# Kernel tuning notes

Measured on AMD Instinct MI355X. Metric: run time of the kernel, lower is better.

## Reference

```python
import jax, jax.numpy as jnp
import numpy as np

NUM_LEVEL = 4

def setup_inputs() -> dict:
    key = jax.random.key(0)
    k1, k2, k3, k4, k5 = jax.random.split(key, 5)
    B, L1, L2, F, H = 8, 1024, 1024, 1024, 1024
    x1_att = jax.random.normal(k1, (B, L1, F), dtype=jnp.float32)
    x2_att = jax.random.normal(k2, (B, L2, F), dtype=jnp.float32)
    x2 = jax.random.normal(k3, (B, L2, H), dtype=jnp.float32)
    x2_mask = jax.random.uniform(k4, (B, L2)) < 0.1
    x2_mask = x2_mask.at[:, 0].set(False)
    W = jax.random.normal(k5, (H, F), dtype=jnp.float32) * 0.02  # nn.Linear weight [out,in]
    final_v = jnp.ones((1, H), dtype=jnp.float32)  # linear_final parameter
    return {"x1_att": x1_att, "x2_att": x2_att, "x2": x2, "x2_mask": x2_mask, "W": W, "final_v": final_v}

def reference(x1_att, x2_att, x2, x2_mask, W, final_v):
    B, L1, F = x1_att.shape
    L2 = x2_att.shape[1]
    H = W.shape[0]
    nl = NUM_LEVEL
    d = H // nl
    # shared linear projection + ReLU (dropout is identity at p=0 / eval)
    x1_key = jax.nn.relu(jnp.einsum('blf,hf->blh', x1_att, W))            # [B,L1,H]
    x2_key = jax.nn.relu(jnp.einsum('blf,hf->blh', x2_att, W)) * final_v  # [B,L2,H]
    x1_rep = x1_key.reshape(B, L1, nl, d)
    x2_rep = x2_key.reshape(B, L2, nl, d)
    # per-level QK^T scores: [B, nl, L1, L2]
    scores = jnp.einsum('bimd,bjmd->bmij', x1_rep, x2_rep)
    scores = jnp.where(x2_mask[:, None, None, :], -jnp.inf, scores)
    alpha = jax.nn.softmax(scores, axis=-1)
    v = x2.reshape(B, L2, nl, d)
    out = jnp.einsum('bmij,bjmd->bimd', alpha, v)  # [B,L1,nl,d]
    return out.reshape(B, L1, H)
```

## Files before the change

kernel.cpp:

```cpp
#include <hip/hip_runtime.h>
#include <hip/hip_bf16.h>
#include <stdint.h>

typedef unsigned short u16;
typedef _Float16 f16_t;
typedef f16_t f16x8 __attribute__((ext_vector_type(8)));
typedef u16 u16x8 __attribute__((ext_vector_type(8)));
typedef u16 u16x4 __attribute__((ext_vector_type(4)));
typedef float f32x4 __attribute__((ext_vector_type(4)));

#define L2E 1.44269504088896f
#define DEFER_THR 7.0f

__device__ __forceinline__ u16 f2h(float f) {
  f16_t h = (f16_t)f;
  return __builtin_bit_cast(u16, h);
}
__device__ __forceinline__ f32x4 mfma16h(u16x8 a, u16x8 b, f32x4 c) {
  return __builtin_amdgcn_mfma_f32_16x16x32_f16(
      __builtin_bit_cast(f16x8, a), __builtin_bit_cast(f16x8, b), c, 0, 0, 0);
}
__device__ __forceinline__ void gl16(const u16 *g, u16 *l) {
  __builtin_amdgcn_global_load_lds(
      (const __attribute__((address_space(1))) void *)g,
      (__attribute__((address_space(3))) void *)l, 16, 0, 0);
}

__global__ void prep_mask_kernel(const unsigned char *__restrict__ mraw,
                                 float *__restrict__ bias) {
  __shared__ int flag;
  int t = threadIdx.x;
  if (t == 0) flag = 0;
  __syncthreads();
  int local = 0;
  for (int i = t; i < 8192; i += 256)
    if ((i & 3) && mraw[i]) local = 1;
  if (local) atomicOr(&flag, 1);
  __syncthreads();
  const bool bytes = (flag != 0);
  const int *mi = (const int *)mraw;
  for (int i = t; i < 8192; i += 256) {
    int m = bytes ? (int)mraw[i] : mi[i];
    bias[i] = m ? -1e30f : 0.0f;
  }
}

__global__ void cvt_f16_kernel(const float *__restrict__ in,
                               u16 *__restrict__ out) {
  int i = (blockIdx.x * 256 + threadIdx.x) * 8;
  f32x4 a = *(const f32x4 *)(in + i);
  f32x4 b = *(const f32x4 *)(in + i + 4);
  u16x8 o;
#pragma unroll
  for (int e = 0; e < 4; ++e) {
    o[e] = f2h(a[e]);
    o[4 + e] = f2h(b[e]);
  }
  *(u16x8 *)(out + i) = o;
}

__global__ void transpose_v_kernel(const float *__restrict__ x2,
                                   u16 *__restrict__ vT) {
  __shared__ float tile[32][33];
  const int b = blockIdx.z, h0 = blockIdx.y * 32, j0 = blockIdx.x * 32;
  const int tx = threadIdx.x & 31, ty = threadIdx.x >> 5;
#pragma unroll
  for (int rr = 0; rr < 32; rr += 8)
    tile[ty + rr][tx] = x2[((size_t)b * 1024 + j0 + ty + rr) * 1024 + h0 + tx];
  __syncthreads();
  const int mlev = h0 >> 8, dd0 = h0 & 255;
#pragma unroll
  for (int rr = 0; rr < 32; rr += 8) {
    int dd = dd0 + ty + rr;
    vT[((size_t)(b * 4 + mlev) * 256 + dd) * 1024 + j0 + tx] =
        f2h(tile[tx][ty + rr]);
  }
}

__global__ __launch_bounds__(256, 2) void proj_kernel(
    const u16 *__restrict__ Ag, const u16 *__restrict__ Bg,
    const float *__restrict__ fv, u16 *__restrict__ outk, int usefv) {
  __shared__ u16 As[2][128 * 32], Bs[2][128 * 32];
  const int t = threadIdx.x;
  const int lane = t & 63, wid = t >> 6;
  const int l16 = lane & 15, g = lane >> 4;
  const int wr = wid >> 1, wc = wid & 1;
  const int bm = blockIdx.x, bn = blockIdx.y;

  f32x4 acc[4][4] = {};

  const int rA0 = 32 * wid + (lane >> 2), rA1 = rA0 + 16;
  const int cA0 = (lane & 3) ^ ((rA0 >> 1) & 3);
  const int cA1 = (lane & 3) ^ ((rA1 >> 1) & 3);
  const u16 *srcA0 = Ag + (size_t)(bm * 128 + rA0) * 1024 + cA0 * 8;
  const u16 *srcA1 = Ag + (size_t)(bm * 128 + rA1) * 1024 + cA1 * 8;
  const u16 *srcB0 = Bg + (size_t)(bn * 128 + rA0) * 1024 + cA0 * 8;
  const u16 *srcB1 = Bg + (size_t)(bn * 128 + rA1) * 1024 + cA1 * 8;
  const int dst0 = wid * 1024, dst1 = wid * 1024 + 512;

  gl16(srcA0, &As[0][dst0]);
  gl16(srcA1, &As[0][dst1]);
  gl16(srcB0, &Bs[0][dst0]);
  gl16(srcB1, &Bs[0][dst1]);

  for (int k0 = 0; k0 < 32; ++k0) {
    const int cur = k0 & 1;
    if (k0 < 31) {
      const int kel = (k0 + 1) * 32, nb = cur ^ 1;
      gl16(srcA0 + kel, &As[nb][dst0]);
      gl16(srcA1 + kel, &As[nb][dst1]);
      gl16(srcB0 + kel, &Bs[nb][dst0]);
      gl16(srcB1 + kel, &Bs[nb][dst1]);
      asm volatile("s_waitcnt vmcnt(4)" ::: "memory");
    } else {
      asm volatile("s_waitcnt vmcnt(0)" ::: "memory");
    }
    __builtin_amdgcn_s_barrier();
    asm volatile("" ::: "memory");

    u16x8 af[4], bf[4];
#pragma unroll
    for (int mf = 0; mf < 4; ++mf) {
      int r = wr * 64 + mf * 16 + l16;
      af[mf] = *(const u16x8 *)(&As[cur][0] + r * 32 + ((g ^ ((r >> 1) & 3)) * 8));
    }
#pragma unroll
    for (int nf = 0; nf < 4; ++nf) {
      int r = wc * 64 + nf * 16 + l16;
      bf[nf] = *(const u16x8 *)(&Bs[cur][0] + r * 32 + ((g ^ ((r >> 1) & 3)) * 8));
    }
    __builtin_amdgcn_s_setprio(1);
#pragma unroll
    for (int mf = 0; mf < 4; ++mf)
#pragma unroll
      for (int nf = 0; nf < 4; ++nf)
        acc[mf][nf] = mfma16h(af[mf], bf[nf], acc[mf][nf]);
    __builtin_amdgcn_s_setprio(0);
    asm volatile("" ::: "memory");
    __builtin_amdgcn_s_barrier();
  }

#pragma unroll
  for (int nf = 0; nf < 4; ++nf) {
    int col = bn * 128 + wc * 64 + nf * 16 + l16;
    float f = usefv ? fv[col] : 1.0f;
#pragma unroll
    for (int mf = 0; mf < 4; ++mf) {
      int row0 = bm * 128 + wr * 64 + mf * 16 + g * 4;
#pragma unroll
      for (int q = 0; q < 4; ++q) {
        float v = acc[mf][nf][q];
        v = (v > 0.f ? v : 0.f) * f;
        outk[(size_t)(row0 + q) * 1024 + col] = f2h(v);
      }
    }
  }
}

__global__ __launch_bounds__(256, 2) void attn_kernel(
    const u16 *__restrict__ x1k, const u16 *__restrict__ x2k,
    const u16 *__restrict__ vT, const float *__restrict__ bias,
    float *__restrict__ out) {
  __shared__ u16 K2s[64 * 256];
  __shared__ u16 VTs[256 * 64];
  __shared__ float biasS[1024];
  __shared__ u16 P[4][16 * 72];

  const int t = threadIdx.x;
  const int lane = t & 63, wid = t >> 6;
  const int l16 = lane & 15, g = lane >> 4;
  const int id = blockIdx.x;
  const int xcd = id & 7, idx = id >> 3;
  const int it = idx & 15, pp = idx >> 4;
  const int pair = xcd + 8 * pp;
  const int b = pair >> 2, m = pair & 3;

  for (int j = t; j < 1024; j += 256) biasS[j] = bias[b * 1024 + j];

  const int qrow = it * 64 + wid * 16 + l16;
  const u16 *qsrc = x1k + ((size_t)b * 1024 + qrow) * 1024 + m * 256;
  u16x8 Q[8];
#pragma unroll
  for (int dk = 0; dk < 8; ++dk) Q[dk] = *(const u16x8 *)(qsrc + dk * 32 + g * 8);

  f32x4 acc[16] = {};
  float mrow[4] = {-1e30f, -1e30f, -1e30f, -1e30f};
  float lrow[4] = {0.f, 0.f, 0.f, 0.f};

  const int sj = t >> 2, cb = (t & 3) * 8;
  const u16 *ksrc = x2k + ((size_t)b * 1024 + sj) * 1024 + m * 256 + cb * 8;
  const u16 *vtsrc = vT + ((size_t)((b * 4 + m) * 256 + t)) * 1024;
  uint32_t koff[8], voff[8];
#pragma unroll
  for (int q = 0; q < 8; ++q) {
    koff[q] = sj * 512 + ((uint32_t)((cb + q) ^ (sj & 7)) << 4);
    voff[q] = t * 128 + ((uint32_t)(q ^ (t & 7)) << 4);
  }

  u16x8 pk[8], pv[8];
#pragma unroll
  for (int q = 0; q < 8; ++q) {
    pk[q] = *(const u16x8 *)(ksrc + q * 8);
    pv[q] = *(const u16x8 *)(vtsrc + q * 8);
  }

  for (int jt = 0; jt < 16; ++jt) {
    __syncthreads();
#pragma unroll
    for (int q = 0; q < 8; ++q) {
      *(u16x8 *)((char *)K2s + koff[q]) = pk[q];
      *(u16x8 *)((char *)VTs + voff[q]) = pv[q];
    }
    __syncthreads();
    if (jt < 15) {
      const u16 *k2 = ksrc + (size_t)(jt + 1) * 64 * 1024;
      const u16 *v2 = vtsrc + (jt + 1) * 64;
#pragma unroll
      for (int q = 0; q < 8; ++q) {
        pk[q] = *(const u16x8 *)(k2 + q * 8);
        pv[q] = *(const u16x8 *)(v2 + q * 8);
      }
    }

    f32x4 s[4] = {};
    __builtin_amdgcn_s_setprio(1);
#pragma unroll
    for (int dk = 0; dk < 8; ++dk) {
#pragma unroll
      for (int jh = 0; jh < 4; ++jh) {
        const int j = jh * 16 + l16;
        uint32_t off = j * 512 + ((uint32_t)((dk * 4 + g) ^ (j & 7)) << 4);
        u16x8 kk = *(const u16x8 *)((const char *)K2s + off);
        s[jh] = mfma16h(Q[dk], kk, s[jh]);
      }
    }
    __builtin_amdgcn_s_setprio(0);

    const int j0 = jt * 64;
    float bj[4];
#pragma unroll
    for (int jh = 0; jh < 4; ++jh) bj[jh] = biasS[j0 + jh * 16 + l16];
    float tm[4];
#pragma unroll
    for (int r = 0; r < 4; ++r) {
#pragma unroll
      for (int jh = 0; jh < 4; ++jh) s[jh][r] += bj[jh];
      tm[r] = fmaxf(fmaxf(s[0][r], s[1][r]), fmaxf(s[2][r], s[3][r]));
    }
#pragma unroll
    for (int d = 1; d < 16; d <<= 1)
#pragma unroll
      for (int r = 0; r < 4; ++r) tm[r] = fmaxf(tm[r], __shfl_xor(tm[r], d, 64));
    bool need = false;
#pragma unroll
    for (int r = 0; r < 4; ++r)
      need = need || ((tm[r] - mrow[r]) * L2E > DEFER_THR);
    if (__any((int)need)) {
#pragma unroll
      for (int r = 0; r < 4; ++r) {
        float nm = fmaxf(mrow[r], tm[r]);
        float sc = exp2f((mrow[r] - nm) * L2E);
        mrow[r] = nm;
        lrow[r] *= sc;
#pragma unroll
        for (int nf = 0; nf < 16; ++nf) acc[nf][r] *= sc;
      }
    }
    float p[4][4], rs[4];
#pragma unroll
    for (int r = 0; r < 4; ++r) {
#pragma unroll
      for (int jh = 0; jh < 4; ++jh) p[jh][r] = exp2f((s[jh][r] - mrow[r]) * L2E);
      rs[r] = (p[0][r] + p[1][r]) + (p[2][r] + p[3][r]);
    }
#pragma unroll
    for (int d = 1; d < 16; d <<= 1)
#pragma unroll
      for (int r = 0; r < 4; ++r) rs[r] += __shfl_xor(rs[r], d, 64);
#pragma unroll
    for (int r = 0; r < 4; ++r) lrow[r] += rs[r];

    u16 *Pw = &P[wid][0];
#pragma unroll
    for (int jh = 0; jh < 4; ++jh)
#pragma unroll
      for (int r = 0; r < 4; ++r)
        Pw[(g * 4 + r) * 72 + jh * 16 + l16] = f2h(p[jh][r]);
    u16x8 pa[2];
#pragma unroll
    for (int kk = 0; kk < 2; ++kk)
      pa[kk] = *(const u16x8 *)(Pw + l16 * 72 + kk * 32 + g * 8);
    __builtin_amdgcn_s_setprio(1);
#pragma unroll
    for (int nf = 0; nf < 16; ++nf) {
      const int dd = nf * 16 + l16;
#pragma unroll
      for (int kk = 0; kk < 2; ++kk) {
        uint32_t off = dd * 128 + ((uint32_t)((kk * 4 + g) ^ (dd & 7)) << 4);
        u16x8 bb = *(const u16x8 *)((const char *)VTs + off);
        acc[nf] = mfma16h(pa[kk], bb, acc[nf]);
      }
    }
    __builtin_amdgcn_s_setprio(0);
  }

  float inv[4];
#pragma unroll
  for (int r = 0; r < 4; ++r) inv[r] = 1.0f / lrow[r];
#pragma unroll
  for (int nf = 0; nf < 16; ++nf) {
    int col = m * 256 + nf * 16 + l16;
#pragma unroll
    for (int r = 0; r < 4; ++r) {
      int row = it * 64 + wid * 16 + g * 4 + r;
      out[((size_t)b * 1024 + row) * 1024 + col] = acc[nf][r] * inv[r];
    }
  }
}

extern "C" void kernel_launch(void *const *d_in, const int *in_sizes, int n_in,
                              void *d_out, int out_size, void *d_ws,
                              size_t ws_size, hipStream_t stream) {
  const float *x1_att = (const float *)d_in[0];
  const float *x2_att = (const float *)d_in[1];
  const float *x2 = (const float *)d_in[2];
  const unsigned char *mask = (const unsigned char *)d_in[3];
  const float *W = (const float *)d_in[4];
  const float *fv = (const float *)d_in[5];
  float *out = (float *)d_out;

  const size_t MB = 1u << 20;
  char *ws = (char *)d_ws;
  u16 *x1a16 = (u16 *)(ws + 0 * MB);
  u16 *x2a16 = (u16 *)(ws + 16 * MB);
  u16 *W16 = (u16 *)(ws + 32 * MB);
  u16 *x1k = (u16 *)(ws + 34 * MB);
  u16 *x2k = (u16 *)(ws + 50 * MB);
  u16 *vT = (u16 *)(ws + 66 * MB);
  float *bias = (float *)(ws + 82 * MB);

  prep_mask_kernel<<<dim3(1), dim3(256), 0, stream>>>(mask, bias);
  cvt_f16_kernel<<<dim3(4096), dim3(256), 0, stream>>>(x1_att, x1a16);
  cvt_f16_kernel<<<dim3(4096), dim3(256), 0, stream>>>(x2_att, x2a16);
  cvt_f16_kernel<<<dim3(512), dim3(256), 0, stream>>>(W, W16);
  proj_kernel<<<dim3(64, 8), dim3(256), 0, stream>>>(x1a16, W16, fv, x1k, 0);
  proj_kernel<<<dim3(64, 8), dim3(256), 0, stream>>>(x2a16, W16, fv, x2k, 1);
  transpose_v_kernel<<<dim3(32, 32, 8), dim3(256), 0, stream>>>(x2, vT);
  attn_kernel<<<dim3(512), dim3(256), 0, stream>>>(x1k, x2k, vT, bias, out);
}
```

Baseline: 323.5 us.

## Deepen projection pipeline to 4 stages and transpose MFMA outputs for vector stores

The projection GEMM moves from a double-buffered to a 4-stage LDS ring with three tiles prefetched ahead, a single barrier per iteration, and no setprio. Both kernels swap the MFMA operand order so each lane holds 4 consecutive columns of one row, which allows 8-byte f16 and 16-byte f32 vectorized global stores in place of scalar strided stores. The attention kernel's per-row rescale and 1/l factors are redistributed with cross-lane shuffles to match the transposed accumulator layout. This uses more LDS in the projection kernel and adds a few shuffles in the online-softmax rescale path.

```diff
diff --git a/kernel.cpp b/kernel.cpp
--- a/kernel.cpp
+++ b/kernel.cpp
@@ -80,7 +80,7 @@
 __global__ __launch_bounds__(256, 2) void proj_kernel(
     const u16 *__restrict__ Ag, const u16 *__restrict__ Bg,
     const float *__restrict__ fv, u16 *__restrict__ outk, int usefv) {
-  __shared__ u16 As[2][128 * 32], Bs[2][128 * 32];
+  __shared__ u16 As[4][128 * 32], Bs[4][128 * 32];
   const int t = threadIdx.x;
   const int lane = t & 63, wid = t >> 6;
   const int l16 = lane & 15, g = lane >> 4;
@@ -98,61 +98,71 @@
   const u16 *srcB1 = Bg + (size_t)(bn * 128 + rA1) * 1024 + cA1 * 8;
   const int dst0 = wid * 1024, dst1 = wid * 1024 + 512;
 
-  gl16(srcA0, &As[0][dst0]);
-  gl16(srcA1, &As[0][dst1]);
-  gl16(srcB0, &Bs[0][dst0]);
-  gl16(srcB1, &Bs[0][dst1]);
+#pragma unroll
+  for (int tt = 0; tt < 3; ++tt) {
+    const int kel = tt * 32;
+    gl16(srcA0 + kel, &As[tt][dst0]);
+    gl16(srcA1 + kel, &As[tt][dst1]);
+    gl16(srcB0 + kel, &Bs[tt][dst0]);
+    gl16(srcB1 + kel, &Bs[tt][dst1]);
+  }
 
   for (int k0 = 0; k0 < 32; ++k0) {
-    const int cur = k0 & 1;
-    if (k0 < 31) {
-      const int kel = (k0 + 1) * 32, nb = cur ^ 1;
+    const int cur = k0 & 3;
+    if (k0 <= 29) {
+      asm volatile("s_waitcnt vmcnt(8)" ::: "memory");
+    } else if (k0 == 30) {
+      asm volatile("s_waitcnt vmcnt(4)" ::: "memory");
+    } else {
+      asm volatile("s_waitcnt vmcnt(0)" ::: "memory");
+    }
+    __builtin_amdgcn_s_barrier();
+    asm volatile("" ::: "memory");
+    if (k0 + 3 < 32) {
+      const int kel = (k0 + 3) * 32, nb = (k0 + 3) & 3;
       gl16(srcA0 + kel, &As[nb][dst0]);
       gl16(srcA1 + kel, &As[nb][dst1]);
       gl16(srcB0 + kel, &Bs[nb][dst0]);
       gl16(srcB1 + kel, &Bs[nb][dst1]);
-      asm volatile("s_waitcnt vmcnt(4)" ::: "memory");
-    } else {
-      asm volatile("s_waitcnt vmcnt(0)" ::: "memory");
-    }
-    __builtin_amdgcn_s_barrier();
-    asm volatile("" ::: "memory");
-
-    u16x8 af[4], bf[4];
-#pragma unroll
-    for (int mf = 0; mf < 4; ++mf) {
-      int r = wr * 64 + mf * 16 + l16;
-      af[mf] = *(const u16x8 *)(&As[cur][0] + r * 32 + ((g ^ ((r >> 1) & 3)) * 8));
-    }
-#pragma unroll
-    for (int nf = 0; nf < 4; ++nf) {
-      int r = wc * 64 + nf * 16 + l16;
-      bf[nf] = *(const u16x8 *)(&Bs[cur][0] + r * 32 + ((g ^ ((r >> 1) & 3)) * 8));
-    }
-    __builtin_amdgcn_s_setprio(1);
-#pragma unroll
-    for (int mf = 0; mf < 4; ++mf)
-#pragma unroll
-      for (int nf = 0; nf < 4; ++nf)
-        acc[mf][nf] = mfma16h(af[mf], bf[nf], acc[mf][nf]);
-    __builtin_amdgcn_s_setprio(0);
-    asm volatile("" ::: "memory");
-    __builtin_amdgcn_s_barrier();
-  }
-
-#pragma unroll
-  for (int nf = 0; nf < 4; ++nf) {
-    int col = bn * 128 + wc * 64 + nf * 16 + l16;
-    float f = usefv ? fv[col] : 1.0f;
-#pragma unroll
-    for (int mf = 0; mf < 4; ++mf) {
-      int row0 = bm * 128 + wr * 64 + mf * 16 + g * 4;
+    }
+
+    u16x8 xf[4], wf[4];
+#pragma unroll
+    for (int mi = 0; mi < 4; ++mi) {
+      int r = wr * 64 + mi * 16 + l16;
+      xf[mi] = *(const u16x8 *)(&As[cur][0] + r * 32 + ((g ^ ((r >> 1) & 3)) * 8));
+    }
+#pragma unroll
+    for (int hi = 0; hi < 4; ++hi) {
+      int r = wc * 64 + hi * 16 + l16;
+      wf[hi] = *(const u16x8 *)(&Bs[cur][0] + r * 32 + ((g ^ ((r >> 1) & 3)) * 8));
+    }
+#pragma unroll
+    for (int hi = 0; hi < 4; ++hi)
+#pragma unroll
+      for (int mi = 0; mi < 4; ++mi)
+        acc[hi][mi] = mfma16h(wf[hi], xf[mi], acc[hi][mi]);
+  }
+
+#pragma unroll
+  for (int hi = 0; hi < 4; ++hi) {
+    const int colbase = bn * 128 + wc * 64 + hi * 16 + g * 4;
+    f32x4 fvv;
+    if (usefv)
+      fvv = *(const f32x4 *)(fv + colbase);
+    else
+      fvv = (f32x4){1.f, 1.f, 1.f, 1.f};
+#pragma unroll
+    for (int mi = 0; mi < 4; ++mi) {
+      const int row = bm * 128 + wr * 64 + mi * 16 + l16;
+      u16x4 o;
 #pragma unroll
       for (int q = 0; q < 4; ++q) {
-        float v = acc[mf][nf][q];
-        v = (v > 0.f ? v : 0.f) * f;
-        outk[(size_t)(row0 + q) * 1024 + col] = f2h(v);
-      }
+        float v = acc[hi][mi][q];
+        v = (v > 0.f ? v : 0.f) * fvv[q];
+        o[q] = f2h(v);
+      }
+      *(u16x4 *)(outk + (size_t)row * 1024 + colbase) = o;
     }
   }
 }
@@ -256,15 +266,23 @@
     for (int r = 0; r < 4; ++r)
       need = need || ((tm[r] - mrow[r]) * L2E > DEFER_THR);
     if (__any((int)need)) {
+      float scv[4];
 #pragma unroll
       for (int r = 0; r < 4; ++r) {
         float nm = fmaxf(mrow[r], tm[r]);
-        float sc = exp2f((mrow[r] - nm) * L2E);
+        scv[r] = exp2f((mrow[r] - nm) * L2E);
         mrow[r] = nm;
-        lrow[r] *= sc;
-#pragma unroll
-        for (int nf = 0; nf < 16; ++nf) acc[nf][r] *= sc;
-      }
+        lrow[r] *= scv[r];
+      }
+      const int src = ((l16 >> 2) << 4) + l16;
+      float s0b = __shfl(scv[0], src, 64), s1b = __shfl(scv[1], src, 64);
+      float s2b = __shfl(scv[2], src, 64), s3b = __shfl(scv[3], src, 64);
+      float scR = (l16 & 2) ? ((l16 & 1) ? s3b : s2b)
+                            : ((l16 & 1) ? s1b : s0b);
+#pragma unroll
+      for (int nf = 0; nf < 16; ++nf)
+#pragma unroll
+        for (int q = 0; q < 4; ++q) acc[nf][q] *= scR;
     }
     float p[4][4], rs[4];
 #pragma unroll
@@ -298,23 +316,27 @@
       for (int kk = 0; kk < 2; ++kk) {
         uint32_t off = dd * 128 + ((uint32_t)((kk * 4 + g) ^ (dd & 7)) << 4);
         u16x8 bb = *(const u16x8 *)((const char *)VTs + off);
-        acc[nf] = mfma16h(pa[kk], bb, acc[nf]);
+        acc[nf] = mfma16h(bb, pa[kk], acc[nf]);
       }
     }
     __builtin_amdgcn_s_setprio(0);
   }
 
-  float inv[4];
-#pragma unroll
-  for (int r = 0; r < 4; ++r) inv[r] = 1.0f / lrow[r];
+  float linv[4];
+#pragma unroll
+  for (int r = 0; r < 4; ++r) linv[r] = 1.0f / lrow[r];
+  const int src = ((l16 >> 2) << 4) + l16;
+  float i0 = __shfl(linv[0], src, 64), i1 = __shfl(linv[1], src, 64);
+  float i2 = __shfl(linv[2], src, 64), i3 = __shfl(linv[3], src, 64);
+  const float invR = (l16 & 2) ? ((l16 & 1) ? i3 : i2) : ((l16 & 1) ? i1 : i0);
+  const int row = it * 64 + wid * 16 + l16;
 #pragma unroll
   for (int nf = 0; nf < 16; ++nf) {
-    int col = m * 256 + nf * 16 + l16;
-#pragma unroll
-    for (int r = 0; r < 4; ++r) {
-      int row = it * 64 + wid * 16 + g * 4 + r;
-      out[((size_t)b * 1024 + row) * 1024 + col] = acc[nf][r] * inv[r];
-    }
+    const int col = m * 256 + nf * 16 + g * 4;
+    f32x4 o;
+#pragma unroll
+    for (int q = 0; q < 4; ++q) o[q] = acc[nf][q] * invR;
+    *(f32x4 *)(out + ((size_t)b * 1024 + row) * 1024 + col) = o;
   }
 }
 
```

New measurement: 328.8 us. Within noise of the previous version (+1.6%).
